# Kernel tuning notes

Hardware: AMD Instinct MI355X
Metric: run time of the kernel (lower is better)

## Reference

```python
import jax, jax.numpy as jnp
import numpy as np

DIM = 768
HEADS = 12
HEAD_DIM = DIM // HEADS
MAX_LEN = 2048
EPS = 1e-5

def layer_norm(x, w, b):
    mu = jnp.mean(x, axis=-1, keepdims=True)
    var = jnp.var(x, axis=-1, keepdims=True)
    return (x - mu) * jax.lax.rsqrt(var + EPS) * w + b


def setup_inputs() -> dict:
    key = jax.random.key(0)
    ks = jax.random.split(key, 16)
    B, N = 2, 2048
    s = 1.0 / np.sqrt(DIM)
    inp = {
        "visible_features": jax.random.normal(ks[0], (B, N, DIM), jnp.float32),
        "infrared_features": jax.random.normal(ks[1], (B, N, DIM), jnp.float32),
        "wq": jax.random.normal(ks[2], (DIM, DIM), jnp.float32) * s,
        "bq": jnp.zeros((DIM,), jnp.float32),
        "lnq_w": jnp.ones((DIM,), jnp.float32),
        "lnq_b": jnp.zeros((DIM,), jnp.float32),
        "wk": jax.random.normal(ks[3], (DIM, DIM), jnp.float32) * s,
        "bk": jnp.zeros((DIM,), jnp.float32),
        "lnk_w": jnp.ones((DIM,), jnp.float32),
        "lnk_b": jnp.zeros((DIM,), jnp.float32),
        "wv": jax.random.normal(ks[4], (DIM, DIM), jnp.float32) * s,
        "bv": jnp.zeros((DIM,), jnp.float32),
        "lnv_w": jnp.ones((DIM,), jnp.float32),
        "lnv_b": jnp.zeros((DIM,), jnp.float32),
        "pos_emb": jax.random.normal(ks[5], (MAX_LEN, DIM), jnp.float32),
        "wo": jax.random.normal(ks[6], (DIM, DIM), jnp.float32) * s,
        "bo": jnp.zeros((DIM,), jnp.float32),
        "gate_w": jax.random.normal(ks[7], (DIM, 2 * DIM), jnp.float32) * (1.0 / np.sqrt(2 * DIM)),
        "gate_b": jnp.zeros((DIM,), jnp.float32),
        "ln_w": jnp.ones((DIM,), jnp.float32),
        "ln_b": jnp.zeros((DIM,), jnp.float32),
    }
    return inp


def reference(visible_features, infrared_features, wq, bq, lnq_w, lnq_b,
              wk, bk, lnk_w, lnk_b, wv, bv, lnv_w, lnv_b,
              pos_emb, wo, bo, gate_w, gate_b, ln_w, ln_b):
    B, N, _ = visible_features.shape
    scale = HEAD_DIM ** -0.5

    def proj_heads(x, w, b, gw, gb):
        y = layer_norm(x @ w.T + b, gw, gb)  # [B,N,D]
        return y.reshape(B, N, HEADS, HEAD_DIM).transpose(0, 2, 1, 3)  # [B,H,N,d]

    q = proj_heads(infrared_features, wq, bq, lnq_w, lnq_b)
    k = proj_heads(visible_features, wk, bk, lnk_w, lnk_b)
    v = proj_heads(visible_features, wv, bv, lnv_w, lnv_b)

    pos = pos_emb[:N].reshape(1, N, HEADS, HEAD_DIM).transpose(0, 2, 1, 3)  # [1,H,N,d]

    scores = jnp.einsum('bhnd,bhmd->bhnm', q, k) * scale
    scores = scores + jnp.einsum('bhnd,xhmd->bhnm', q, pos)
    attn = jax.nn.softmax(scores, axis=-1)  # dropout is identity in eval

    out = jnp.einsum('bhnm,bhmd->bhnd', attn, v)
    out = out.transpose(0, 2, 1, 3).reshape(B, N, DIM)
    out = out @ wo.T + bo

    gate = jax.nn.sigmoid(jnp.concatenate([visible_features, out], axis=-1) @ gate_w.T + gate_b)
    fused = visible_features * gate + out * (1.0 - gate)
    return layer_norm(fused, ln_w, ln_b)
```

## Files before the change

### kernel.cpp

```cpp
#include <hip/hip_runtime.h>
#include <hip/hip_bf16.h>

#define DIMC 768
#define NSEQ 2048
#define NB 2
#define NH 12
#define HD 64
#define EPSLN 1e-5f
#define LOG2E 1.44269504f

typedef __attribute__((ext_vector_type(8))) short          bf16x8;
typedef __attribute__((ext_vector_type(8))) unsigned short ushort8;
typedef __attribute__((ext_vector_type(4))) unsigned short ushort4v;
typedef __attribute__((ext_vector_type(4))) float          f32x4;
typedef unsigned int u32;

__device__ __forceinline__ unsigned short f2b(float f) {
    union { float f; unsigned u; } x; x.f = f;
    unsigned r = x.u + 0x7fffu + ((x.u >> 16) & 1u);
    return (unsigned short)(r >> 16);
}
__device__ __forceinline__ float b2f(unsigned short v) {
    union { unsigned u; float f; } x; x.u = ((u32)v) << 16; return x.f;
}

#define MFMA16(a, b, c) __builtin_amdgcn_mfma_f32_16x16x32_bf16((a), (b), (c), 0, 0, 0)

__device__ __forceinline__ void gl_lds16(const unsigned short* g, unsigned short* l) {
    __builtin_amdgcn_global_load_lds(
        (const __attribute__((address_space(1))) u32*)(const void*)g,
        (__attribute__((address_space(3))) u32*)(void*)l, 16, 0, 0);
}

#define G_WQ   147456
#define G_MW   442368
#define G_G2   147456
#define G_WO   147456
#define G_VIS  786432
#define G_INF  786432
#define G_BF_TOTAL (G_WQ + G_MW + G_G2 + G_WO + G_VIS + G_INF)
#define G_BIAS 576
#define G_ALL  (G_BF_TOTAL + G_BIAS)

__global__ __launch_bounds__(256)
void cast_all_kernel(const float* __restrict__ wq, const float* __restrict__ wk,
                     const float* __restrict__ wv, const float* __restrict__ gw,
                     const float* __restrict__ wo,
                     const float* __restrict__ bk, const float* __restrict__ bv,
                     const float* __restrict__ gb,
                     const float* __restrict__ vis, const float* __restrict__ inf_,
                     unsigned short* __restrict__ o_wq, unsigned short* __restrict__ o_mw,
                     unsigned short* __restrict__ o_g2, unsigned short* __restrict__ o_wo,
                     unsigned short* __restrict__ o_vis, unsigned short* __restrict__ o_inf,
                     float* __restrict__ o_biasc)
{
    const int g = blockIdx.x * 256 + threadIdx.x;
    if (g >= G_ALL) return;
    if (g >= G_BF_TOTAL) {
        const int e0 = (g - G_BF_TOTAL) * 4;
        float4 r;
        float* pr = (float*)&r;
        #pragma unroll
        for (int t = 0; t < 4; ++t) {
            const int e = e0 + t;
            pr[t] = (e < 768) ? bk[e] : (e < 1536) ? bv[e - 768] : gb[e - 1536];
        }
        *(float4*)&o_biasc[e0] = r;
        return;
    }
    const float* src; unsigned short* dst; int soff, doff = 0;
    int gg = g;
    if (gg < G_WQ) { src = wq; dst = o_wq; soff = gg; doff = gg; }
    else if ((gg -= G_WQ) < G_MW) {
        const int row = gg / 192, c4 = gg % 192;
        dst = o_mw; doff = gg;
        if      (row < 768)  { src = wk; soff = row * 192 + c4; }
        else if (row < 1536) { src = wv; soff = (row - 768) * 192 + c4; }
        else                 { src = gw; soff = (row - 1536) * 384 + c4; }
    }
    else if ((gg -= G_MW) < G_G2) {
        const int row = gg / 192, c4 = gg % 192;
        src = gw; soff = row * 384 + 192 + c4; dst = o_g2; doff = gg;
    }
    else if ((gg -= G_G2) < G_WO)  { src = wo;   dst = o_wo;  soff = gg; doff = gg; }
    else if ((gg -= G_WO) < G_VIS) { src = vis;  dst = o_vis; soff = gg; doff = gg; }
    else { gg -= G_VIS;              src = inf_; dst = o_inf; soff = gg; doff = gg; }
    f32x4 v = ((const f32x4*)src)[soff];
    ushort4v t;
    t[0] = f2b(v[0]); t[1] = f2b(v[1]); t[2] = f2b(v[2]); t[3] = f2b(v[3]);
    ((ushort4v*)dst)[doff] = t;
}

template<int MODE>
__global__ __launch_bounds__(256)
void gemm128x64(const unsigned short* __restrict__ A,
                const unsigned short* __restrict__ W,
                const float* __restrict__ bias,
                float* __restrict__ Cf,
                unsigned short* __restrict__ Cb)
{
    __shared__ unsigned short As[2][128 * 64];
    __shared__ unsigned short Bs[2][64 * 64];
    const int m0 = blockIdx.x * 128, n0 = blockIdx.y * 64;
    const int lane = threadIdx.x & 63, wid = threadIdx.x >> 6;
    const int wm = wid >> 1, wn = wid & 1;
    const int r16 = lane & 15, kg = lane >> 4;
    const int lr = lane >> 3, lc = (lane & 7) * 8;

    f32x4 acc[4][2] = {};

    auto stage = [&](int k0, int buf) {
        #pragma unroll
        for (int i = 0; i < 4; ++i) {
            const int c = wid * 4 + i;
            gl_lds16(&A[(size_t)(m0 + c * 8 + lr) * DIMC + k0 + lc], &As[buf][c * 512]);
        }
        #pragma unroll
        for (int i = 0; i < 2; ++i) {
            const int c = wid * 2 + i;
            gl_lds16(&W[(size_t)(n0 + c * 8 + lr) * DIMC + k0 + lc], &Bs[buf][c * 512]);
        }
    };

    stage(0, 0);
    for (int t = 0; t < 12; ++t) {
        const int cur = t & 1;
        if (t < 11) {
            stage((t + 1) * 64, cur ^ 1);
            asm volatile("s_waitcnt vmcnt(6)" ::: "memory");
        } else {
            asm volatile("s_waitcnt vmcnt(0)" ::: "memory");
        }
        __builtin_amdgcn_s_barrier();
        __builtin_amdgcn_sched_barrier(0);
        #pragma unroll
        for (int ks = 0; ks < 2; ++ks) {
            bf16x8 af[4], bg[2];
            #pragma unroll
            for (int mi = 0; mi < 4; ++mi)
                af[mi] = *(const bf16x8*)&As[cur][(wm * 64 + mi * 16 + r16) * 64 + ks * 32 + kg * 8];
            #pragma unroll
            for (int nj = 0; nj < 2; ++nj)
                bg[nj] = *(const bf16x8*)&Bs[cur][(wn * 32 + nj * 16 + r16) * 64 + ks * 32 + kg * 8];
            __builtin_amdgcn_s_setprio(1);
            #pragma unroll
            for (int mi = 0; mi < 4; ++mi)
                #pragma unroll
                for (int nj = 0; nj < 2; ++nj)
                    acc[mi][nj] = MFMA16(af[mi], bg[nj], acc[mi][nj]);
            __builtin_amdgcn_s_setprio(0);
        }
        __builtin_amdgcn_sched_barrier(0);
        __builtin_amdgcn_s_barrier();
    }

    #pragma unroll
    for (int mi = 0; mi < 4; ++mi)
    #pragma unroll
    for (int nj = 0; nj < 2; ++nj) {
        const int gr = m0 + wm * 64 + mi * 16 + kg * 4;
        const int gc = n0 + wn * 32 + nj * 16 + r16;
        const float bvl = (MODE == 3) ? 0.f : bias[gc];
        #pragma unroll
        for (int r = 0; r < 4; ++r) {
            const float val = acc[mi][nj][r] + bvl;
            if (MODE == 0) {
                Cf[(size_t)(gr + r) * DIMC + gc] = val;
            } else if (MODE == 1) {
                if (gc < 1536) Cb[(size_t)(gr + r) * 1536 + gc] = f2b(val);
                else           Cf[(size_t)(gr + r) * DIMC + (gc - 1536)] = val;
            } else if (MODE == 2) {
                const size_t idx = (size_t)(gr + r) * DIMC + gc;
                Cf[idx] = val;
                Cb[idx] = f2b(val);
            } else {
                const size_t idx = (size_t)(gr + r) * DIMC + gc;
                Cf[idx] += val;
            }
        }
    }
}

template<int INBF, int MODE>
__global__ __launch_bounds__(256)
void ln_bf16_kernel(const void* __restrict__ Zv,
                    int ld,
                    const float* __restrict__ w,
                    const float* __restrict__ b,
                    const float* __restrict__ pos,
                    unsigned short* __restrict__ out)
{
    const int row = blockIdx.x;
    const int n = row & (NSEQ - 1);
    float x[3];
    float s = 0.f, q = 0.f;
    #pragma unroll
    for (int u = 0; u < 3; ++u) {
        const int j = threadIdx.x + u * 256;
        if (INBF) x[u] = b2f(((const unsigned short*)Zv)[(size_t)row * ld + j]);
        else      x[u] = ((const float*)Zv)[(size_t)row * ld + j];
        s += x[u];
        q += x[u] * x[u];
    }
    #pragma unroll
    for (int off = 32; off > 0; off >>= 1) {
        s += __shfl_down(s, off);
        q += __shfl_down(q, off);
    }
    __shared__ float ls[8];
    const int wv_ = threadIdx.x >> 6;
    if ((threadIdx.x & 63) == 0) { ls[wv_] = s; ls[4 + wv_] = q; }
    __syncthreads();
    if (threadIdx.x == 0) {
        ls[0] = ls[0] + ls[1] + ls[2] + ls[3];
        ls[4] = ls[4] + ls[5] + ls[6] + ls[7];
    }
    __syncthreads();
    const float mu  = ls[0] * (1.f / DIMC);
    const float var = ls[4] * (1.f / DIMC) - mu * mu;
    const float rs  = rsqrtf(var + EPSLN);
    #pragma unroll
    for (int u = 0; u < 3; ++u) {
        const int j = threadIdx.x + u * 256;
        float y = (x[u] - mu) * rs * w[j] + b[j];
        if (MODE == 1) y = y * (0.125f * LOG2E) + pos[(size_t)n * DIMC + j] * LOG2E;
        out[(size_t)row * DIMC + j] = f2b(y);
    }
}

__global__ __launch_bounds__(256)
void attn_bf16_kernel(const unsigned short* __restrict__ Q,
                      const unsigned short* __restrict__ K,
                      const unsigned short* __restrict__ V,
                      unsigned short* __restrict__ O)
{
    __shared__ unsigned short Ks[64][72];
    __shared__ unsigned short Vt[64][72];
    __shared__ unsigned short Ps[4][32][72];

    const int bh = blockIdx.x;
    const int b = bh / NH, h = bh % NH;
    const int n0 = blockIdx.y * 128;
    const int lane = threadIdx.x & 63, w = threadIdx.x >> 6;
    const int r16 = lane & 15, kg = lane >> 4;

    const size_t base = (size_t)b * NSEQ * DIMC + (size_t)h * HD;

    bf16x8 aq[2][2];
    #pragma unroll
    for (int qf = 0; qf < 2; ++qf) {
        const size_t qo = base + (size_t)(n0 + w * 32 + qf * 16 + r16) * DIMC + kg * 8;
        aq[qf][0] = *(const bf16x8*)&Q[qo];
        aq[qf][1] = *(const bf16x8*)&Q[qo + 32];
    }

    const int krow = threadIdx.x >> 2;
    const int kcol = (threadIdx.x & 3) * 16;
    const unsigned short* Kg = K + base + (size_t)krow * DIMC + kcol;
    const int vrow = threadIdx.x & 63;
    const int vcol = (threadIdx.x >> 6) * 16;
    const unsigned short* Vg = V + base + (size_t)vrow * DIMC + vcol;

    f32x4 o[2][4] = {};
    float m_run[2] = {-1e30f, -1e30f};
    float l_run[2] = {0.f, 0.f};

    ushort8  kr0 = *(const ushort8*)Kg;
    ushort8  kr1 = *(const ushort8*)(Kg + 8);
    ushort4v vr[4];
    #pragma unroll
    for (int i = 0; i < 4; ++i) vr[i] = *(const ushort4v*)(Vg + i * 4);
    *(ushort8*)&Ks[krow][kcol]     = kr0;
    *(ushort8*)&Ks[krow][kcol + 8] = kr1;
    #pragma unroll
    for (int i = 0; i < 4; ++i)
        #pragma unroll
        for (int e = 0; e < 4; ++e)
            Vt[vcol + i * 4 + e][vrow] = vr[i][e];
    __syncthreads();

    for (int m0 = 0; m0 < NSEQ; m0 += 64) {
        const bool more = (m0 + 64 < NSEQ);
        if (more) {
            const size_t adv = (size_t)(m0 + 64) * DIMC;
            kr0 = *(const ushort8*)(Kg + adv);
            kr1 = *(const ushort8*)(Kg + adv + 8);
            #pragma unroll
            for (int i = 0; i < 4; ++i) vr[i] = *(const ushort4v*)(Vg + adv + i * 4);
        }
        __builtin_amdgcn_sched_barrier(0);

        f32x4 sv[4][2];
        #pragma unroll
        for (int f = 0; f < 4; ++f)
            #pragma unroll
            for (int qf = 0; qf < 2; ++qf)
                sv[f][qf] = (f32x4){0.f, 0.f, 0.f, 0.f};
        __builtin_amdgcn_s_setprio(1);
        #pragma unroll
        for (int f = 0; f < 4; ++f) {
            bf16x8 kb0 = *(const bf16x8*)&Ks[f * 16 + r16][kg * 8];
            bf16x8 kb1 = *(const bf16x8*)&Ks[f * 16 + r16][32 + kg * 8];
            #pragma unroll
            for (int qf = 0; qf < 2; ++qf) {
                sv[f][qf] = MFMA16(kb0, aq[qf][0], sv[f][qf]);
                sv[f][qf] = MFMA16(kb1, aq[qf][1], sv[f][qf]);
            }
        }
        __builtin_amdgcn_s_setprio(0);

        float mt[2];
        #pragma unroll
        for (int qf = 0; qf < 2; ++qf) {
            float m = sv[0][qf][0];
            #pragma unroll
            for (int f = 0; f < 4; ++f)
                #pragma unroll
                for (int j = 0; j < 4; ++j)
                    m = fmaxf(m, sv[f][qf][j]);
            m = fmaxf(m, __shfl_xor(m, 16));
            m = fmaxf(m, __shfl_xor(m, 32));
            mt[qf] = m;
        }
        const float growth = fmaxf(mt[0] - m_run[0], mt[1] - m_run[1]);
        const bool defer = __all(growth <= 8.0f);
        float corr[2] = {1.f, 1.f};
        if (!defer) {
            #pragma unroll
            for (int qf = 0; qf < 2; ++qf) {
                const float mn = fmaxf(m_run[qf], mt[qf]);
                corr[qf] = exp2f(m_run[qf] - mn);
                m_run[qf] = mn;
            }
        }

        #pragma unroll
        for (int qf = 0; qf < 2; ++qf) {
            float st = 0.f;
            #pragma unroll
            for (int f = 0; f < 4; ++f) {
                float p0 = exp2f(sv[f][qf][0] - m_run[qf]);
                float p1 = exp2f(sv[f][qf][1] - m_run[qf]);
                float p2 = exp2f(sv[f][qf][2] - m_run[qf]);
                float p3 = exp2f(sv[f][qf][3] - m_run[qf]);
                st += (p0 + p1) + (p2 + p3);
                u32 w0, w1;
                asm("v_cvt_pk_bf16_f32 %0, %1, %2" : "=v"(w0) : "v"(p0), "v"(p1));
                asm("v_cvt_pk_bf16_f32 %0, %1, %2" : "=v"(w1) : "v"(p2), "v"(p3));
                *(u32*)&Ps[w][qf * 16 + r16][f * 16 + kg * 4]     = w0;
                *(u32*)&Ps[w][qf * 16 + r16][f * 16 + kg * 4 + 2] = w1;
            }
            st += __shfl_xor(st, 16);
            st += __shfl_xor(st, 32);
            l_run[qf] = l_run[qf] * corr[qf] + st;
        }

        if (!defer) {
            #pragma unroll
            for (int ri = 0; ri < 2; ++ri)
                #pragma unroll
                for (int jj = 0; jj < 4; ++jj) {
                    const float cq = __shfl(corr[ri], kg * 4 + jj);
                    #pragma unroll
                    for (int nj = 0; nj < 4; ++nj) o[ri][nj][jj] *= cq;
                }
        }

        __builtin_amdgcn_s_setprio(1);
        #pragma unroll
        for (int ri = 0; ri < 2; ++ri) {
            bf16x8 pa0 = *(const bf16x8*)&Ps[w][ri * 16 + r16][kg * 8];
            bf16x8 pa1 = *(const bf16x8*)&Ps[w][ri * 16 + r16][32 + kg * 8];
            #pragma unroll
            for (int nj = 0; nj < 4; ++nj) {
                bf16x8 vb0 = *(const bf16x8*)&Vt[nj * 16 + r16][kg * 8];
                bf16x8 vb1 = *(const bf16x8*)&Vt[nj * 16 + r16][32 + kg * 8];
                o[ri][nj] = MFMA16(pa0, vb0, o[ri][nj]);
                o[ri][nj] = MFMA16(pa1, vb1, o[ri][nj]);
            }
        }
        __builtin_amdgcn_s_setprio(0);

        __builtin_amdgcn_s_barrier();
        __builtin_amdgcn_sched_barrier(0);
        if (more) {
            *(ushort8*)&Ks[krow][kcol]     = kr0;
            *(ushort8*)&Ks[krow][kcol + 8] = kr1;
            #pragma unroll
            for (int i = 0; i < 4; ++i)
                #pragma unroll
                for (int e = 0; e < 4; ++e)
                    Vt[vcol + i * 4 + e][vrow] = vr[i][e];
        }
        __syncthreads();
    }

    float rinv[2];
    rinv[0] = 1.f / l_run[0];
    rinv[1] = 1.f / l_run[1];
    #pragma unroll
    for (int ri = 0; ri < 2; ++ri)
        #pragma unroll
        for (int jj = 0; jj < 4; ++jj) {
            const float cq = __shfl(rinv[ri], kg * 4 + jj);
            #pragma unroll
            for (int nj = 0; nj < 4; ++nj) {
                const size_t go = base + (size_t)(n0 + w * 32 + ri * 16 + kg * 4 + jj) * DIMC
                                + nj * 16 + r16;
                O[go] = f2b(o[ri][nj][jj] * cq);
            }
        }
}

__global__ __launch_bounds__(256)
void fuse_ln_kernel(const float* __restrict__ vis,
                    const float* __restrict__ Oc,
                    const float* __restrict__ G,
                    const float* __restrict__ w,
                    const float* __restrict__ b,
                    float* __restrict__ out)
{
    const int row = blockIdx.x;
    float f[3];
    float s = 0.f, q = 0.f;
    #pragma unroll
    for (int u = 0; u < 3; ++u) {
        const size_t idx = (size_t)row * DIMC + threadIdx.x + u * 256;
        const float vv = vis[idx];
        const float oo = Oc[idx];
        const float gg = 1.f / (1.f + __expf(-G[idx]));
        f[u] = vv * gg + oo * (1.f - gg);
        s += f[u];
        q += f[u] * f[u];
    }
    #pragma unroll
    for (int off = 32; off > 0; off >>= 1) {
        s += __shfl_down(s, off);
        q += __shfl_down(q, off);
    }
    __shared__ float ls[8];
    const int wv_ = threadIdx.x >> 6;
    if ((threadIdx.x & 63) == 0) { ls[wv_] = s; ls[4 + wv_] = q; }
    __syncthreads();
    if (threadIdx.x == 0) {
        ls[0] = ls[0] + ls[1] + ls[2] + ls[3];
        ls[4] = ls[4] + ls[5] + ls[6] + ls[7];
    }
    __syncthreads();
    const float mu  = ls[0] * (1.f / DIMC);
    const float var = ls[4] * (1.f / DIMC) - mu * mu;
    const float rs  = rsqrtf(var + EPSLN);
    #pragma unroll
    for (int u = 0; u < 3; ++u) {
        const int j = threadIdx.x + u * 256;
        out[(size_t)row * DIMC + j] = (f[u] - mu) * rs * w[j] + b[j];
    }
}

extern "C" void kernel_launch(void* const* d_in, const int* in_sizes, int n_in,
                              void* d_out, int out_size, void* d_ws, size_t ws_size,
                              hipStream_t stream)
{
    const float* vis  = (const float*)d_in[0];
    const float* inf_ = (const float*)d_in[1];
    const float* wq   = (const float*)d_in[2];
    const float* bq   = (const float*)d_in[3];
    const float* lnqw = (const float*)d_in[4];
    const float* lnqb = (const float*)d_in[5];
    const float* wk   = (const float*)d_in[6];
    const float* bk   = (const float*)d_in[7];
    const float* lnkw = (const float*)d_in[8];
    const float* lnkb = (const float*)d_in[9];
    const float* wv   = (const float*)d_in[10];
    const float* bv   = (const float*)d_in[11];
    const float* lnvw = (const float*)d_in[12];
    const float* lnvb = (const float*)d_in[13];
    const float* pos  = (const float*)d_in[14];
    const float* wo   = (const float*)d_in[15];
    const float* bo   = (const float*)d_in[16];
    const float* gw   = (const float*)d_in[17];
    const float* gb   = (const float*)d_in[18];
    const float* lnw  = (const float*)d_in[19];
    const float* lnb  = (const float*)d_in[20];

    const size_t WEL = 589824;
    const size_t MWEL = 1769472;
    const size_t BUF = (size_t)NB * NSEQ * DIMC;

    unsigned short* p = (unsigned short*)d_ws;
    unsigned short* wq_b  = p;  p += WEL;
    unsigned short* mw_b  = p;  p += MWEL;
    unsigned short* g2_b  = p;  p += WEL;
    unsigned short* wo_b  = p;  p += WEL;
    unsigned short* vis_b = p;  p += BUF;
    unsigned short* inf_b = p;  p += BUF;
    unsigned short* q_b   = p;  p += BUF;
    unsigned short* k_b   = p;  p += BUF;
    unsigned short* v_b   = p;  p += BUF;
    unsigned short* kvpre = p;  p += 2 * BUF;
    float* biasc = (float*)p;

    float* Gd  = (float*)d_out;
    float* Oc  = (float*)k_b;
    unsigned short* oc_b = inf_b;

    dim3 blk(256);

    cast_all_kernel<<<dim3((G_ALL + 255) / 256), blk, 0, stream>>>(
        wq, wk, wv, gw, wo, bk, bv, gb, vis, inf_,
        wq_b, mw_b, g2_b, wo_b, vis_b, inf_b, biasc);

    gemm128x64<0><<<dim3(32, 12), blk, 0, stream>>>(inf_b, wq_b, bq, Gd, nullptr);
    ln_bf16_kernel<0, 0><<<dim3(4096), blk, 0, stream>>>(Gd, DIMC, lnqw, lnqb, nullptr, q_b);

    gemm128x64<1><<<dim3(32, 36), blk, 0, stream>>>(vis_b, mw_b, biasc, Gd, kvpre);
    ln_bf16_kernel<1, 1><<<dim3(4096), blk, 0, stream>>>(kvpre, 1536, lnkw, lnkb, pos, k_b);
    ln_bf16_kernel<1, 0><<<dim3(4096), blk, 0, stream>>>(kvpre + DIMC, 1536, lnvw, lnvb, nullptr, v_b);

    attn_bf16_kernel<<<dim3(NB * NH, NSEQ / 128), blk, 0, stream>>>(q_b, k_b, v_b, q_b);

    gemm128x64<2><<<dim3(32, 12), blk, 0, stream>>>(q_b, wo_b, bo, Oc, oc_b);

    gemm128x64<3><<<dim3(32, 12), blk, 0, stream>>>(oc_b, g2_b, nullptr, Gd, nullptr);

    fuse_ln_kernel<<<dim3(4096), blk, 0, stream>>>(vis, Oc, Gd, lnw, lnb, (float*)d_out);
}
```

Before: 314.0 us.

## Merge projection GEMMs, fold Wo into gate weights, retile attention to 64-query blocks

Puts the Q, KV-gate and W2 = G2·Wo GEMMs into one grouped launch with a swizzled block order. It precomputes a combined bias and concatenates the Wo and W2 weights, so the output projection and the gate's out-half become a single GEMM. The layernorm kernels are merged, and Q/K/V pre-activations are now stored as bf16. Attention now uses 64-query blocks with 128-key tiles and occupancy bound 3 to get more blocks and fewer loop iterations. The Wo-folding adds a weight-weight GEMM and a strided transpose write in the cast kernel. It also uses wo_b as the concatenated [Wo;W2] weight, which relies on W2 sitting directly after wo_b in the workspace.

```diff
diff --git a/kernel.cpp b/kernel.cpp
--- a/kernel.cpp
+++ b/kernel.cpp
@@ -13,6 +13,7 @@
 typedef __attribute__((ext_vector_type(8))) unsigned short ushort8;
 typedef __attribute__((ext_vector_type(4))) unsigned short ushort4v;
 typedef __attribute__((ext_vector_type(4))) float          f32x4;
+typedef __attribute__((ext_vector_type(2))) unsigned int   u32x2;
 typedef unsigned int u32;
 
 __device__ __forceinline__ unsigned short f2b(float f) {
@@ -51,6 +52,7 @@
                      const float* __restrict__ vis, const float* __restrict__ inf_,
                      unsigned short* __restrict__ o_wq, unsigned short* __restrict__ o_mw,
                      unsigned short* __restrict__ o_g2, unsigned short* __restrict__ o_wo,
+                     unsigned short* __restrict__ o_wot,
                      unsigned short* __restrict__ o_vis, unsigned short* __restrict__ o_inf,
                      float* __restrict__ o_biasc)
 {
@@ -69,6 +71,7 @@
         return;
     }
     const float* src; unsigned short* dst; int soff, doff = 0;
+    bool is_wo = false; int wor = 0, woc = 0;
     int gg = g;
     if (gg < G_WQ) { src = wq; dst = o_wq; soff = gg; doff = gg; }
     else if ((gg -= G_WQ) < G_MW) {
@@ -82,43 +85,61 @@
         const int row = gg / 192, c4 = gg % 192;
         src = gw; soff = row * 384 + 192 + c4; dst = o_g2; doff = gg;
     }
-    else if ((gg -= G_G2) < G_WO)  { src = wo;   dst = o_wo;  soff = gg; doff = gg; }
+    else if ((gg -= G_G2) < G_WO) {
+        src = wo; dst = o_wo; soff = gg; doff = gg;
+        is_wo = true; wor = gg / 192; woc = (gg % 192) * 4;
+    }
     else if ((gg -= G_WO) < G_VIS) { src = vis;  dst = o_vis; soff = gg; doff = gg; }
     else { gg -= G_VIS;              src = inf_; dst = o_inf; soff = gg; doff = gg; }
     f32x4 v = ((const f32x4*)src)[soff];
     ushort4v t;
     t[0] = f2b(v[0]); t[1] = f2b(v[1]); t[2] = f2b(v[2]); t[3] = f2b(v[3]);
     ((ushort4v*)dst)[doff] = t;
-}
-
-template<int MODE>
+    if (is_wo) {
+        #pragma unroll
+        for (int e = 0; e < 4; ++e)
+            o_wot[(size_t)(woc + e) * DIMC + wor] = t[e];
+    }
+}
+
 __global__ __launch_bounds__(256)
-void gemm128x64(const unsigned short* __restrict__ A,
-                const unsigned short* __restrict__ W,
-                const float* __restrict__ bias,
-                float* __restrict__ Cf,
-                unsigned short* __restrict__ Cb)
-{
-    __shared__ unsigned short As[2][128 * 64];
-    __shared__ unsigned short Bs[2][64 * 64];
-    const int m0 = blockIdx.x * 128, n0 = blockIdx.y * 64;
+void bias2_kernel(const float* __restrict__ gw, const float* __restrict__ bo,
+                  float* __restrict__ biasc2)
+{
+    const int i = blockIdx.x * 256 + threadIdx.x;
+    if (i >= 768) return;
+    biasc2[i] = bo[i];
+    const float* row = gw + (size_t)i * 1536 + 768;
+    float s = 0.f;
+    for (int k = 0; k < 768; k += 4) {
+        float4 gv = *(const float4*)&row[k];
+        float4 bv = *(const float4*)&bo[k];
+        s += gv.x * bv.x + gv.y * bv.y + gv.z * bv.z + gv.w * bv.w;
+    }
+    biasc2[768 + i] = s;
+}
+
+__device__ __forceinline__ void gemm_core(const unsigned short* __restrict__ A,
+                                          const unsigned short* __restrict__ W,
+                                          int m0, int n0,
+                                          unsigned short* As, unsigned short* Bs,
+                                          f32x4 (&acc)[4][2])
+{
     const int lane = threadIdx.x & 63, wid = threadIdx.x >> 6;
     const int wm = wid >> 1, wn = wid & 1;
     const int r16 = lane & 15, kg = lane >> 4;
     const int lr = lane >> 3, lc = (lane & 7) * 8;
 
-    f32x4 acc[4][2] = {};
-
     auto stage = [&](int k0, int buf) {
         #pragma unroll
         for (int i = 0; i < 4; ++i) {
             const int c = wid * 4 + i;
-            gl_lds16(&A[(size_t)(m0 + c * 8 + lr) * DIMC + k0 + lc], &As[buf][c * 512]);
+            gl_lds16(&A[(size_t)(m0 + c * 8 + lr) * DIMC + k0 + lc], &As[buf * 8192 + c * 512]);
         }
         #pragma unroll
         for (int i = 0; i < 2; ++i) {
             const int c = wid * 2 + i;
-            gl_lds16(&W[(size_t)(n0 + c * 8 + lr) * DIMC + k0 + lc], &Bs[buf][c * 512]);
+            gl_lds16(&W[(size_t)(n0 + c * 8 + lr) * DIMC + k0 + lc], &Bs[buf * 4096 + c * 512]);
         }
     };
 
@@ -138,10 +159,10 @@
             bf16x8 af[4], bg[2];
             #pragma unroll
             for (int mi = 0; mi < 4; ++mi)
-                af[mi] = *(const bf16x8*)&As[cur][(wm * 64 + mi * 16 + r16) * 64 + ks * 32 + kg * 8];
+                af[mi] = *(const bf16x8*)&As[cur * 8192 + (wm * 64 + mi * 16 + r16) * 64 + ks * 32 + kg * 8];
             #pragma unroll
             for (int nj = 0; nj < 2; ++nj)
-                bg[nj] = *(const bf16x8*)&Bs[cur][(wn * 32 + nj * 16 + r16) * 64 + ks * 32 + kg * 8];
+                bg[nj] = *(const bf16x8*)&Bs[cur * 4096 + (wn * 32 + nj * 16 + r16) * 64 + ks * 32 + kg * 8];
             __builtin_amdgcn_s_setprio(1);
             #pragma unroll
             for (int mi = 0; mi < 4; ++mi)
@@ -153,52 +174,102 @@
         __builtin_amdgcn_sched_barrier(0);
         __builtin_amdgcn_s_barrier();
     }
-
+}
+
+__global__ __launch_bounds__(256)
+void gemm_p1(const unsigned short* __restrict__ inf_b, const unsigned short* __restrict__ vis_b,
+             const unsigned short* __restrict__ g2_b,  const unsigned short* __restrict__ wq_b,
+             const unsigned short* __restrict__ mw_b,  const unsigned short* __restrict__ wo_t,
+             const float* __restrict__ bq, const float* __restrict__ biasc,
+             unsigned short* __restrict__ qpre,
+             unsigned short* __restrict__ k_b, unsigned short* __restrict__ v_b,
+             float* __restrict__ Gd, unsigned short* __restrict__ W2)
+{
+    __shared__ unsigned short As[2 * 8192];
+    __shared__ unsigned short Bs[2 * 4096];
+    int bid = (int)blockIdx.x;
+    bid = (bid & 7) * 201 + (bid >> 3);
+    const unsigned short *A, *W;
+    int m0, n0, sub;
+    if (bid < 384)       { sub = 0; const int b = bid;        m0 = (b / 12) * 128; n0 = (b % 12) * 64; A = inf_b; W = wq_b; }
+    else if (bid < 1536) { sub = 1; const int b = bid - 384;  m0 = (b / 36) * 128; n0 = (b % 36) * 64; A = vis_b; W = mw_b; }
+    else                 { sub = 2; const int b = bid - 1536; m0 = (b / 12) * 128; n0 = (b % 12) * 64; A = g2_b;  W = wo_t; }
+
+    f32x4 acc[4][2] = {};
+    gemm_core(A, W, m0, n0, As, Bs, acc);
+
+    const int lane = threadIdx.x & 63, wid = threadIdx.x >> 6;
+    const int wm = wid >> 1, wn = wid & 1;
+    const int r16 = lane & 15, kg = lane >> 4;
     #pragma unroll
     for (int mi = 0; mi < 4; ++mi)
     #pragma unroll
     for (int nj = 0; nj < 2; ++nj) {
-        const int gr = m0 + wm * 64 + mi * 16 + kg * 4;
-        const int gc = n0 + wn * 32 + nj * 16 + r16;
-        const float bvl = (MODE == 3) ? 0.f : bias[gc];
+        const int gr0 = m0 + wm * 64 + mi * 16 + kg * 4;
+        const int gc  = n0 + wn * 32 + nj * 16 + r16;
         #pragma unroll
         for (int r = 0; r < 4; ++r) {
-            const float val = acc[mi][nj][r] + bvl;
-            if (MODE == 0) {
-                Cf[(size_t)(gr + r) * DIMC + gc] = val;
-            } else if (MODE == 1) {
-                if (gc < 1536) Cb[(size_t)(gr + r) * 1536 + gc] = f2b(val);
-                else           Cf[(size_t)(gr + r) * DIMC + (gc - 1536)] = val;
-            } else if (MODE == 2) {
-                const size_t idx = (size_t)(gr + r) * DIMC + gc;
-                Cf[idx] = val;
-                Cb[idx] = f2b(val);
+            const int gr = gr0 + r;
+            float val = acc[mi][nj][r];
+            if (sub == 0) {
+                qpre[(size_t)gr * DIMC + gc] = f2b(val + bq[gc]);
+            } else if (sub == 1) {
+                val += biasc[gc];
+                if      (gc < 768)  k_b[(size_t)gr * DIMC + gc] = f2b(val);
+                else if (gc < 1536) v_b[(size_t)gr * DIMC + (gc - 768)] = f2b(val);
+                else                Gd[(size_t)gr * DIMC + (gc - 1536)] = val;
             } else {
-                const size_t idx = (size_t)(gr + r) * DIMC + gc;
-                Cf[idx] += val;
+                W2[(size_t)gr * DIMC + gc] = f2b(val);
             }
         }
     }
 }
 
-template<int INBF, int MODE>
 __global__ __launch_bounds__(256)
-void ln_bf16_kernel(const void* __restrict__ Zv,
-                    int ld,
-                    const float* __restrict__ w,
-                    const float* __restrict__ b,
-                    const float* __restrict__ pos,
-                    unsigned short* __restrict__ out)
+void gemm_p2(const unsigned short* __restrict__ ao_b, const unsigned short* __restrict__ wo_cat,
+             const float* __restrict__ biasc2,
+             float* __restrict__ Oc, float* __restrict__ Gd)
+{
+    __shared__ unsigned short As[2 * 8192];
+    __shared__ unsigned short Bs[2 * 4096];
+    int bid = (int)blockIdx.x;
+    bid = (bid & 7) * 96 + (bid >> 3);
+    const int m0 = (bid / 24) * 128, n0 = (bid % 24) * 64;
+
+    f32x4 acc[4][2] = {};
+    gemm_core(ao_b, wo_cat, m0, n0, As, Bs, acc);
+
+    const int lane = threadIdx.x & 63, wid = threadIdx.x >> 6;
+    const int wm = wid >> 1, wn = wid & 1;
+    const int r16 = lane & 15, kg = lane >> 4;
+    #pragma unroll
+    for (int mi = 0; mi < 4; ++mi)
+    #pragma unroll
+    for (int nj = 0; nj < 2; ++nj) {
+        const int gr0 = m0 + wm * 64 + mi * 16 + kg * 4;
+        const int gc  = n0 + wn * 32 + nj * 16 + r16;
+        #pragma unroll
+        for (int r = 0; r < 4; ++r) {
+            const int gr = gr0 + r;
+            const float val = acc[mi][nj][r] + biasc2[gc];
+            if (gc < 768) Oc[(size_t)gr * DIMC + gc] = val;
+            else          Gd[(size_t)gr * DIMC + (gc - 768)] += val;
+        }
+    }
+}
+
+__global__ __launch_bounds__(256)
+void ln_q_kernel(const unsigned short* __restrict__ Z,
+                 const float* __restrict__ w, const float* __restrict__ b,
+                 unsigned short* __restrict__ out)
 {
     const int row = blockIdx.x;
-    const int n = row & (NSEQ - 1);
     float x[3];
     float s = 0.f, q = 0.f;
     #pragma unroll
     for (int u = 0; u < 3; ++u) {
         const int j = threadIdx.x + u * 256;
-        if (INBF) x[u] = b2f(((const unsigned short*)Zv)[(size_t)row * ld + j]);
-        else      x[u] = ((const float*)Zv)[(size_t)row * ld + j];
+        x[u] = b2f(Z[(size_t)row * DIMC + j]);
         s += x[u];
         q += x[u] * x[u];
     }
@@ -222,194 +293,214 @@
     #pragma unroll
     for (int u = 0; u < 3; ++u) {
         const int j = threadIdx.x + u * 256;
+        out[(size_t)row * DIMC + j] = f2b((x[u] - mu) * rs * w[j] + b[j]);
+    }
+}
+
+__global__ __launch_bounds__(256)
+void ln_kv_kernel(const float* __restrict__ lnkw, const float* __restrict__ lnkb,
+                  const float* __restrict__ lnvw, const float* __restrict__ lnvb,
+                  const float* __restrict__ pos,
+                  unsigned short* __restrict__ k_b, unsigned short* __restrict__ v_b)
+{
+    const int bid = blockIdx.x;
+    const bool isK = bid < 4096;
+    const int row = bid & 4095;
+    const int n = row & (NSEQ - 1);
+    unsigned short* buf = (isK ? k_b : v_b) + (size_t)row * DIMC;
+    const float* w = isK ? lnkw : lnvw;
+    const float* b = isK ? lnkb : lnvb;
+
+    float x[3];
+    float s = 0.f, q = 0.f;
+    #pragma unroll
+    for (int u = 0; u < 3; ++u) {
+        const int j = threadIdx.x + u * 256;
+        x[u] = b2f(buf[j]);
+        s += x[u];
+        q += x[u] * x[u];
+    }
+    #pragma unroll
+    for (int off = 32; off > 0; off >>= 1) {
+        s += __shfl_down(s, off);
+        q += __shfl_down(q, off);
+    }
+    __shared__ float ls[8];
+    const int wv_ = threadIdx.x >> 6;
+    if ((threadIdx.x & 63) == 0) { ls[wv_] = s; ls[4 + wv_] = q; }
+    __syncthreads();
+    if (threadIdx.x == 0) {
+        ls[0] = ls[0] + ls[1] + ls[2] + ls[3];
+        ls[4] = ls[4] + ls[5] + ls[6] + ls[7];
+    }
+    __syncthreads();
+    const float mu  = ls[0] * (1.f / DIMC);
+    const float var = ls[4] * (1.f / DIMC) - mu * mu;
+    const float rs  = rsqrtf(var + EPSLN);
+    #pragma unroll
+    for (int u = 0; u < 3; ++u) {
+        const int j = threadIdx.x + u * 256;
         float y = (x[u] - mu) * rs * w[j] + b[j];
-        if (MODE == 1) y = y * (0.125f * LOG2E) + pos[(size_t)n * DIMC + j] * LOG2E;
-        out[(size_t)row * DIMC + j] = f2b(y);
-    }
-}
-
-__global__ __launch_bounds__(256)
+        if (isK) y = y * (0.125f * LOG2E) + pos[(size_t)n * DIMC + j] * LOG2E;
+        buf[j] = f2b(y);
+    }
+}
+
+__global__ __launch_bounds__(256, 3)
 void attn_bf16_kernel(const unsigned short* __restrict__ Q,
                       const unsigned short* __restrict__ K,
                       const unsigned short* __restrict__ V,
                       unsigned short* __restrict__ O)
 {
-    __shared__ unsigned short Ks[64][72];
-    __shared__ unsigned short Vt[64][72];
-    __shared__ unsigned short Ps[4][32][72];
+    __shared__ unsigned short Ks[128][72];
+    __shared__ unsigned short Vt[64][136];
+    __shared__ unsigned short Ps[4][16][136];
 
     const int bh = blockIdx.x;
     const int b = bh / NH, h = bh % NH;
-    const int n0 = blockIdx.y * 128;
-    const int lane = threadIdx.x & 63, w = threadIdx.x >> 6;
+    const int n0 = blockIdx.y * 64;
+    const int tid = threadIdx.x;
+    const int lane = tid & 63, w = tid >> 6;
     const int r16 = lane & 15, kg = lane >> 4;
 
     const size_t base = (size_t)b * NSEQ * DIMC + (size_t)h * HD;
 
-    bf16x8 aq[2][2];
-    #pragma unroll
-    for (int qf = 0; qf < 2; ++qf) {
-        const size_t qo = base + (size_t)(n0 + w * 32 + qf * 16 + r16) * DIMC + kg * 8;
-        aq[qf][0] = *(const bf16x8*)&Q[qo];
-        aq[qf][1] = *(const bf16x8*)&Q[qo + 32];
-    }
-
-    const int krow = threadIdx.x >> 2;
-    const int kcol = (threadIdx.x & 3) * 16;
+    const size_t qoff = base + (size_t)(n0 + w * 16 + r16) * DIMC + kg * 8;
+    bf16x8 aq0 = *(const bf16x8*)&Q[qoff];
+    bf16x8 aq1 = *(const bf16x8*)&Q[qoff + 32];
+
+    const int krow = tid >> 1;
+    const int kcol = (tid & 1) * 32;
     const unsigned short* Kg = K + base + (size_t)krow * DIMC + kcol;
-    const int vrow = threadIdx.x & 63;
-    const int vcol = (threadIdx.x >> 6) * 16;
-    const unsigned short* Vg = V + base + (size_t)vrow * DIMC + vcol;
-
-    f32x4 o[2][4] = {};
-    float m_run[2] = {-1e30f, -1e30f};
-    float l_run[2] = {0.f, 0.f};
-
-    ushort8  kr0 = *(const ushort8*)Kg;
-    ushort8  kr1 = *(const ushort8*)(Kg + 8);
-    ushort4v vr[4];
-    #pragma unroll
-    for (int i = 0; i < 4; ++i) vr[i] = *(const ushort4v*)(Vg + i * 4);
-    *(ushort8*)&Ks[krow][kcol]     = kr0;
-    *(ushort8*)&Ks[krow][kcol + 8] = kr1;
-    #pragma unroll
-    for (int i = 0; i < 4; ++i)
-        #pragma unroll
-        for (int e = 0; e < 4; ++e)
-            Vt[vcol + i * 4 + e][vrow] = vr[i][e];
+    const int vkv = lane;
+    const int vdc = w * 16;
+    const unsigned short* Vg = V + base + (size_t)vkv * DIMC + vdc;
+
+    f32x4 o[4] = {};
+    float m_run = -1e30f, l_run = 0.f;
+
+    ushort8 pk[4];
+    ushort8 pv[2][2];
+
+    auto pf_load = [&](size_t adv) {
+        #pragma unroll
+        for (int i = 0; i < 4; ++i) pk[i] = *(const ushort8*)(Kg + adv + 8 * i);
+        #pragma unroll
+        for (int rep = 0; rep < 2; ++rep)
+            #pragma unroll
+            for (int hh = 0; hh < 2; ++hh)
+                pv[rep][hh] = *(const ushort8*)(Vg + adv + (size_t)rep * 64 * DIMC + hh * 8);
+    };
+    auto pf_write = [&]() {
+        #pragma unroll
+        for (int i = 0; i < 4; ++i) *(ushort8*)&Ks[krow][kcol + 8 * i] = pk[i];
+        #pragma unroll
+        for (int rep = 0; rep < 2; ++rep)
+            #pragma unroll
+            for (int hh = 0; hh < 2; ++hh)
+                #pragma unroll
+                for (int e = 0; e < 8; ++e)
+                    Vt[vdc + hh * 8 + e][vkv + rep * 64] = pv[rep][hh][e];
+    };
+
+    pf_load(0);
+    pf_write();
     __syncthreads();
 
-    for (int m0 = 0; m0 < NSEQ; m0 += 64) {
-        const bool more = (m0 + 64 < NSEQ);
-        if (more) {
-            const size_t adv = (size_t)(m0 + 64) * DIMC;
-            kr0 = *(const ushort8*)(Kg + adv);
-            kr1 = *(const ushort8*)(Kg + adv + 8);
-            #pragma unroll
-            for (int i = 0; i < 4; ++i) vr[i] = *(const ushort4v*)(Vg + adv + i * 4);
-        }
+    for (int m0 = 0; m0 < NSEQ; m0 += 128) {
+        const bool more = (m0 + 128 < NSEQ);
+        if (more) pf_load((size_t)(m0 + 128) * DIMC);
         __builtin_amdgcn_sched_barrier(0);
 
-        f32x4 sv[4][2];
-        #pragma unroll
-        for (int f = 0; f < 4; ++f)
-            #pragma unroll
-            for (int qf = 0; qf < 2; ++qf)
-                sv[f][qf] = (f32x4){0.f, 0.f, 0.f, 0.f};
+        f32x4 sv[8];
+        #pragma unroll
+        for (int f = 0; f < 8; ++f) sv[f] = (f32x4){0.f, 0.f, 0.f, 0.f};
         __builtin_amdgcn_s_setprio(1);
         #pragma unroll
-        for (int f = 0; f < 4; ++f) {
+        for (int f = 0; f < 8; ++f) {
             bf16x8 kb0 = *(const bf16x8*)&Ks[f * 16 + r16][kg * 8];
             bf16x8 kb1 = *(const bf16x8*)&Ks[f * 16 + r16][32 + kg * 8];
-            #pragma unroll
-            for (int qf = 0; qf < 2; ++qf) {
-                sv[f][qf] = MFMA16(kb0, aq[qf][0], sv[f][qf]);
-                sv[f][qf] = MFMA16(kb1, aq[qf][1], sv[f][qf]);
-            }
+            sv[f] = MFMA16(kb0, aq0, sv[f]);
+            sv[f] = MFMA16(kb1, aq1, sv[f]);
         }
         __builtin_amdgcn_s_setprio(0);
 
-        float mt[2];
-        #pragma unroll
-        for (int qf = 0; qf < 2; ++qf) {
-            float m = sv[0][qf][0];
-            #pragma unroll
-            for (int f = 0; f < 4; ++f)
-                #pragma unroll
-                for (int j = 0; j < 4; ++j)
-                    m = fmaxf(m, sv[f][qf][j]);
-            m = fmaxf(m, __shfl_xor(m, 16));
-            m = fmaxf(m, __shfl_xor(m, 32));
-            mt[qf] = m;
-        }
-        const float growth = fmaxf(mt[0] - m_run[0], mt[1] - m_run[1]);
-        const bool defer = __all(growth <= 8.0f);
-        float corr[2] = {1.f, 1.f};
+        float mf[8];
+        #pragma unroll
+        for (int f = 0; f < 8; ++f)
+            mf[f] = fmaxf(fmaxf(sv[f][0], sv[f][1]), fmaxf(sv[f][2], sv[f][3]));
+        float m01 = fmaxf(mf[0], mf[1]), m23 = fmaxf(mf[2], mf[3]);
+        float m45 = fmaxf(mf[4], mf[5]), m67 = fmaxf(mf[6], mf[7]);
+        float mt = fmaxf(fmaxf(m01, m23), fmaxf(m45, m67));
+        mt = fmaxf(mt, __shfl_xor(mt, 16));
+        mt = fmaxf(mt, __shfl_xor(mt, 32));
+
+        const bool defer = __all(mt - m_run <= 8.0f);
+        float corr = 1.f;
+        if (!defer) {
+            const float mn = fmaxf(m_run, mt);
+            corr = exp2f(m_run - mn);
+            m_run = mn;
+        }
+
+        float sf[8];
+        #pragma unroll
+        for (int f = 0; f < 8; ++f) {
+            float p0 = exp2f(sv[f][0] - m_run);
+            float p1 = exp2f(sv[f][1] - m_run);
+            float p2 = exp2f(sv[f][2] - m_run);
+            float p3 = exp2f(sv[f][3] - m_run);
+            sf[f] = (p0 + p1) + (p2 + p3);
+            u32 w0, w1;
+            asm("v_cvt_pk_bf16_f32 %0, %1, %2" : "=v"(w0) : "v"(p0), "v"(p1));
+            asm("v_cvt_pk_bf16_f32 %0, %1, %2" : "=v"(w1) : "v"(p2), "v"(p3));
+            u32x2 pw; pw[0] = w0; pw[1] = w1;
+            *(u32x2*)&Ps[w][r16][f * 16 + kg * 4] = pw;
+        }
+        float st = ((sf[0] + sf[1]) + (sf[2] + sf[3])) + ((sf[4] + sf[5]) + (sf[6] + sf[7]));
+        st += __shfl_xor(st, 16);
+        st += __shfl_xor(st, 32);
+        l_run = l_run * corr + st;
+
         if (!defer) {
             #pragma unroll
-            for (int qf = 0; qf < 2; ++qf) {
-                const float mn = fmaxf(m_run[qf], mt[qf]);
-                corr[qf] = exp2f(m_run[qf] - mn);
-                m_run[qf] = mn;
+            for (int jj = 0; jj < 4; ++jj) {
+                const float cq = __shfl(corr, kg * 4 + jj);
+                o[0][jj] *= cq; o[1][jj] *= cq; o[2][jj] *= cq; o[3][jj] *= cq;
             }
         }
 
-        #pragma unroll
-        for (int qf = 0; qf < 2; ++qf) {
-            float st = 0.f;
+        bf16x8 pa[4];
+        #pragma unroll
+        for (int s = 0; s < 4; ++s)
+            pa[s] = *(const bf16x8*)&Ps[w][r16][s * 32 + kg * 8];
+        __builtin_amdgcn_s_setprio(1);
+        #pragma unroll
+        for (int nj = 0; nj < 4; ++nj) {
             #pragma unroll
-            for (int f = 0; f < 4; ++f) {
-                float p0 = exp2f(sv[f][qf][0] - m_run[qf]);
-                float p1 = exp2f(sv[f][qf][1] - m_run[qf]);
-                float p2 = exp2f(sv[f][qf][2] - m_run[qf]);
-                float p3 = exp2f(sv[f][qf][3] - m_run[qf]);
-                st += (p0 + p1) + (p2 + p3);
-                u32 w0, w1;
-                asm("v_cvt_pk_bf16_f32 %0, %1, %2" : "=v"(w0) : "v"(p0), "v"(p1));
-                asm("v_cvt_pk_bf16_f32 %0, %1, %2" : "=v"(w1) : "v"(p2), "v"(p3));
-                *(u32*)&Ps[w][qf * 16 + r16][f * 16 + kg * 4]     = w0;
-                *(u32*)&Ps[w][qf * 16 + r16][f * 16 + kg * 4 + 2] = w1;
-            }
-            st += __shfl_xor(st, 16);
-            st += __shfl_xor(st, 32);
-            l_run[qf] = l_run[qf] * corr[qf] + st;
-        }
-
-        if (!defer) {
-            #pragma unroll
-            for (int ri = 0; ri < 2; ++ri)
-                #pragma unroll
-                for (int jj = 0; jj < 4; ++jj) {
-                    const float cq = __shfl(corr[ri], kg * 4 + jj);
-                    #pragma unroll
-                    for (int nj = 0; nj < 4; ++nj) o[ri][nj][jj] *= cq;
-                }
-        }
-
-        __builtin_amdgcn_s_setprio(1);
-        #pragma unroll
-        for (int ri = 0; ri < 2; ++ri) {
-            bf16x8 pa0 = *(const bf16x8*)&Ps[w][ri * 16 + r16][kg * 8];
-            bf16x8 pa1 = *(const bf16x8*)&Ps[w][ri * 16 + r16][32 + kg * 8];
-            #pragma unroll
-            for (int nj = 0; nj < 4; ++nj) {
-                bf16x8 vb0 = *(const bf16x8*)&Vt[nj * 16 + r16][kg * 8];
-                bf16x8 vb1 = *(const bf16x8*)&Vt[nj * 16 + r16][32 + kg * 8];
-                o[ri][nj] = MFMA16(pa0, vb0, o[ri][nj]);
-                o[ri][nj] = MFMA16(pa1, vb1, o[ri][nj]);
+            for (int s = 0; s < 4; ++s) {
+                bf16x8 vb = *(const bf16x8*)&Vt[nj * 16 + r16][s * 32 + kg * 8];
+                o[nj] = MFMA16(pa[s], vb, o[nj]);
             }
         }
         __builtin_amdgcn_s_setprio(0);
 
         __builtin_amdgcn_s_barrier();
         __builtin_amdgcn_sched_barrier(0);
-        if (more) {
-            *(ushort8*)&Ks[krow][kcol]     = kr0;
-            *(ushort8*)&Ks[krow][kcol + 8] = kr1;
-            #pragma unroll
-            for (int i = 0; i < 4; ++i)
-                #pragma unroll
-                for (int e = 0; e < 4; ++e)
-                    Vt[vcol + i * 4 + e][vrow] = vr[i][e];
-        }
+        if (more) pf_write();
         __syncthreads();
     }
 
-    float rinv[2];
-    rinv[0] = 1.f / l_run[0];
-    rinv[1] = 1.f / l_run[1];
-    #pragma unroll
-    for (int ri = 0; ri < 2; ++ri)
-        #pragma unroll
-        for (int jj = 0; jj < 4; ++jj) {
-            const float cq = __shfl(rinv[ri], kg * 4 + jj);
-            #pragma unroll
-            for (int nj = 0; nj < 4; ++nj) {
-                const size_t go = base + (size_t)(n0 + w * 32 + ri * 16 + kg * 4 + jj) * DIMC
-                                + nj * 16 + r16;
-                O[go] = f2b(o[ri][nj][jj] * cq);
-            }
-        }
+    const float linv = 1.f / l_run;
+    #pragma unroll
+    for (int jj = 0; jj < 4; ++jj) {
+        const float cq = __shfl(linv, kg * 4 + jj);
+        #pragma unroll
+        for (int nj = 0; nj < 4; ++nj) {
+            const size_t go = base + (size_t)(n0 + w * 16 + kg * 4 + jj) * DIMC + nj * 16 + r16;
+            O[go] = f2b(o[nj][jj] * cq);
+        }
+    }
 }
 
 __global__ __launch_bounds__(256)
@@ -488,40 +579,40 @@
     const size_t BUF = (size_t)NB * NSEQ * DIMC;
 
     unsigned short* p = (unsigned short*)d_ws;
-    unsigned short* wq_b  = p;  p += WEL;
-    unsigned short* mw_b  = p;  p += MWEL;
-    unsigned short* g2_b  = p;  p += WEL;
-    unsigned short* wo_b  = p;  p += WEL;
-    unsigned short* vis_b = p;  p += BUF;
-    unsigned short* inf_b = p;  p += BUF;
-    unsigned short* q_b   = p;  p += BUF;
-    unsigned short* k_b   = p;  p += BUF;
-    unsigned short* v_b   = p;  p += BUF;
-    unsigned short* kvpre = p;  p += 2 * BUF;
-    float* biasc = (float*)p;
-
-    float* Gd  = (float*)d_out;
-    float* Oc  = (float*)k_b;
-    unsigned short* oc_b = inf_b;
+    unsigned short* wq_b   = p;  p += WEL;
+    unsigned short* mw_b   = p;  p += MWEL;
+    unsigned short* g2_b   = p;  p += WEL;
+    unsigned short* wo_b   = p;  p += WEL;
+    unsigned short* W2     = p;  p += WEL;
+    unsigned short* wo_t   = p;  p += WEL;
+    unsigned short* vis_b  = p;  p += BUF;
+    unsigned short* inf_b  = p;  p += BUF;
+    unsigned short* qpre_b = p;  p += BUF;
+    unsigned short* q_b    = p;  p += BUF;
+    unsigned short* k_b    = p;  p += BUF;
+    unsigned short* v_b    = p;  p += BUF;
+    float* biasc  = (float*)p;  p += 4608;
+    float* biasc2 = (float*)p;  p += 3072;
+
+    float* Gd = (float*)d_out;
+    float* Oc = (float*)k_b;
 
     dim3 blk(256);
 
+    bias2_kernel<<<dim3(3), blk, 0, stream>>>(gw, bo, biasc2);
     cast_all_kernel<<<dim3((G_ALL + 255) / 256), blk, 0, stream>>>(
         wq, wk, wv, gw, wo, bk, bv, gb, vis, inf_,
-        wq_b, mw_b, g2_b, wo_b, vis_b, inf_b, biasc);
-
-    gemm128x64<0><<<dim3(32, 12), blk, 0, stream>>>(inf_b, wq_b, bq, Gd, nullptr);
-    ln_bf16_kernel<0, 0><<<dim3(4096), blk, 0, stream>>>(Gd, DIMC, lnqw, lnqb, nullptr, q_b);
-
-    gemm128x64<1><<<dim3(32, 36), blk, 0, stream>>>(vis_b, mw_b, biasc, Gd, kvpre);
-    ln_bf16_kernel<1, 1><<<dim3(4096), blk, 0, stream>>>(kvpre, 1536, lnkw, lnkb, pos, k_b);
-    ln_bf16_kernel<1, 0><<<dim3(4096), blk, 0, stream>>>(kvpre + DIMC, 1536, lnvw, lnvb, nullptr, v_b);
-
-    attn_bf16_kernel<<<dim3(NB * NH, NSEQ / 128), blk, 0, stream>>>(q_b, k_b, v_b, q_b);
-
-    gemm128x64<2><<<dim3(32, 12), blk, 0, stream>>>(q_b, wo_b, bo, Oc, oc_b);
-
-    gemm128x64<3><<<dim3(32, 12), blk, 0, stream>>>(oc_b, g2_b, nullptr, Gd, nullptr);
+        wq_b, mw_b, g2_b, wo_b, wo_t, vis_b, inf_b, biasc);
+
+    gemm_p1<<<dim3(1608), blk, 0, stream>>>(inf_b, vis_b, g2_b, wq_b, mw_b, wo_t,
+                                            bq, biasc, qpre_b, k_b, v_b, Gd, W2);
+
+    ln_q_kernel<<<dim3(4096), blk, 0, stream>>>(qpre_b, lnqw, lnqb, q_b);
+    ln_kv_kernel<<<dim3(8192), blk, 0, stream>>>(lnkw, lnkb, lnvw, lnvb, pos, k_b, v_b);
+
+    attn_bf16_kernel<<<dim3(NB * NH, NSEQ / 64), blk, 0, stream>>>(q_b, k_b, v_b, q_b);
+
+    gemm_p2<<<dim3(768), blk, 0, stream>>>(q_b, wo_b, biasc2, Oc, Gd);
 
     fuse_ln_kernel<<<dim3(4096), blk, 0, stream>>>(vis, Oc, Gd, lnw, lnb, (float*)d_out);
 }
```

After: 328.5 us. 4.6% more time.
